# Kernel tuning notes

Hardware: AMD Instinct MI355X
Metric: run time of the kernel (lower is better)

Reference implementation:

```python
import jax, jax.numpy as jnp
import numpy as np
from jax import lax

STRIDE, PADDING, DILATION = 1, 1, 1


def setup_inputs() -> dict:
    key = jax.random.key(0)
    ks = jax.random.split(key, 6)
    B, C, H, W = 32, 128, 64, 64
    K, O, ksz = 4, 256, 3
    red = 32  # C // reduction
    # kaiming-ish scales
    return {
        "x": jax.random.normal(ks[0], (B, C, H, W), jnp.float32),
        "weights": jax.random.normal(ks[1], (K, O, C, ksz, ksz), jnp.float32) * (1.0 / np.sqrt(C * ksz * ksz)),
        "w1": jax.random.normal(ks[2], (red, C), jnp.float32) * (1.0 / np.sqrt(C)),
        "b1": jnp.zeros((red,), jnp.float32),
        "w2": jax.random.normal(ks[3], (K, red), jnp.float32) * (1.0 / np.sqrt(red)),
        "b2": jnp.zeros((K,), jnp.float32),
    }


def reference(x, weights, w1, b1, w2, b2):
    B, C, H, W = x.shape
    K, O, Cw, kh, kw = weights.shape
    # attention over kernels: global avg pool -> MLP -> softmax  [B, K]
    pooled = jnp.mean(x, axis=(2, 3))                       # [B, C]
    h = jax.nn.relu(pooled @ w1.T + b1)                     # [B, red]
    att = jax.nn.softmax(h @ w2.T + b2, axis=1)             # [B, K]
    # per-sample mixed kernel: [B, O, C, kh, kw]
    wk = jnp.einsum('bk,koihw->boihw', att, weights)
    # batched per-sample conv via grouped convolution (groups = B)
    lhs = x.reshape(1, B * C, H, W)
    rhs = wk.reshape(B * O, C, kh, kw)
    out = lax.conv_general_dilated(
        lhs, rhs,
        window_strides=(STRIDE, STRIDE),
        padding=[(PADDING, PADDING), (PADDING, PADDING)],
        rhs_dilation=(DILATION, DILATION),
        dimension_numbers=('NCHW', 'OIHW', 'NCHW'),
        feature_group_count=B,
    )
    Ho, Wo = out.shape[2], out.shape[3]
    return out.reshape(B, O, Ho, Wo)
```

## Files before the change

### kernel.cpp

```cpp
#include <hip/hip_runtime.h>
#include <math.h>

#define BB 32
#define CC 128
#define HH 64
#define WW 64
#define KK 4
#define OO 256
#define RED 32
#define HWSZ (HH*WW)
#define XT_W 66
#define GPLANE (XT_W*XT_W)

typedef __attribute__((ext_vector_type(8))) short bf16x8;
typedef __attribute__((ext_vector_type(4))) float f32x4;

static __device__ __forceinline__ unsigned short f2bf(float f) {
    unsigned int u = __float_as_uint(f);
    u += 0x7FFF + ((u >> 16) & 1);
    return (unsigned short)(u >> 16);
}

static __device__ __forceinline__ void async16(unsigned short* lds, const unsigned short* g) {
    __builtin_amdgcn_global_load_lds(
        (const __attribute__((address_space(1))) unsigned int*)g,
        (__attribute__((address_space(3))) unsigned int*)lds, 16, 0, 0);
}

__global__ __launch_bounds__(256) void transpose_pool(const float* __restrict__ x,
        unsigned short* __restrict__ xt, float* __restrict__ partial) {
    __shared__ float lt[CC][65];
    int h = blockIdx.x & 63;
    int b = blockIdx.x >> 6;
    const float* xb = x + ((size_t)b * CC * HH + h) * WW;
    for (int i = threadIdx.x; i < CC * 16; i += 256) {
        int c = i >> 4, f4 = i & 15;
        float4 v = *(const float4*)(xb + (size_t)c * HWSZ + f4 * 4);
        lt[c][f4 * 4 + 0] = v.x;
        lt[c][f4 * 4 + 1] = v.y;
        lt[c][f4 * 4 + 2] = v.z;
        lt[c][f4 * 4 + 3] = v.w;
    }
    __syncthreads();
    size_t bg = (size_t)b * 4;
    for (int i = threadIdx.x; i < 64 * 16; i += 256) {
        int ww = i >> 4, cs = i & 15;
        bf16x8 pk;
#pragma unroll
        for (int j = 0; j < 8; ++j) pk[j] = (short)f2bf(lt[cs * 8 + j][ww]);
        *(bf16x8*)&xt[(((bg + (cs >> 2)) * XT_W + (h + 1)) * XT_W + (ww + 1)) * 32 + (cs & 3) * 8] = pk;
    }
    if (threadIdx.x < 32) {
        int cs = threadIdx.x & 15;
        int col = (threadIdx.x < 16) ? 0 : 65;
        *(f32x4*)&xt[(((bg + (cs >> 2)) * XT_W + (h + 1)) * XT_W + col) * 32 + (cs & 3) * 8] =
            (f32x4){0.f, 0.f, 0.f, 0.f};
    }
    if (h == 0 || h == 63) {
        int hr = (h == 0) ? 0 : 65;
        for (int i = threadIdx.x; i < XT_W * 16; i += 256) {
            int px = i >> 4, cs = i & 15;
            *(f32x4*)&xt[(((bg + (cs >> 2)) * XT_W + hr) * XT_W + px) * 32 + (cs & 3) * 8] =
                (f32x4){0.f, 0.f, 0.f, 0.f};
        }
    }
    if (threadIdx.x < CC) {
        float s = 0.f;
#pragma unroll
        for (int j = 0; j < WW; ++j) s += lt[threadIdx.x][j];
        partial[(size_t)blockIdx.x * CC + threadIdx.x] = s;
    }
}

__global__ void att_kernel(const float* __restrict__ partial,
        const float* __restrict__ w1, const float* __restrict__ b1,
        const float* __restrict__ w2, const float* __restrict__ b2,
        float* __restrict__ att) {
    int b = blockIdx.x;
    int tid = threadIdx.x;
    __shared__ float ps[CC];
    __shared__ float hs[RED];
    __shared__ float ls[KK];
    if (tid < CC) {
        const float* pp = partial + (size_t)b * HH * CC + tid;
        float s = 0.f;
#pragma unroll
        for (int h = 0; h < HH; ++h) s += pp[(size_t)h * CC];
        ps[tid] = s * (1.0f / (float)HWSZ);
    }
    __syncthreads();
    int r = tid >> 3, j = tid & 7;
    const float* w1r = w1 + r * CC + j * 16;
    float p = 0.f;
#pragma unroll
    for (int c = 0; c < 16; ++c) p = fmaf(ps[j * 16 + c], w1r[c], p);
    p += __shfl_xor(p, 1, 64);
    p += __shfl_xor(p, 2, 64);
    p += __shfl_xor(p, 4, 64);
    if (j == 0) hs[r] = fmaxf(p + b1[r], 0.f);
    __syncthreads();
    if (tid < KK) {
        float acc = b2[tid];
        const float* w2k = w2 + tid * RED;
#pragma unroll
        for (int rr = 0; rr < RED; ++rr) acc = fmaf(hs[rr], w2k[rr], acc);
        ls[tid] = acc;
    }
    __syncthreads();
    if (tid == 0) {
        float m = fmaxf(fmaxf(ls[0], ls[1]), fmaxf(ls[2], ls[3]));
        float e0 = expf(ls[0] - m), e1 = expf(ls[1] - m);
        float e2 = expf(ls[2] - m), e3 = expf(ls[3] - m);
        float inv = 1.0f / (e0 + e1 + e2 + e3);
        att[b * KK + 0] = e0 * inv; att[b * KK + 1] = e1 * inv;
        att[b * KK + 2] = e2 * inv; att[b * KK + 3] = e3 * inv;
    }
}

__global__ __launch_bounds__(256) void mix_kernel(const float* __restrict__ w,
        const float* __restrict__ att, unsigned short* __restrict__ wk) {
    int gid = blockIdx.x * 256 + threadIdx.x;
    int c = gid & 127;
    int o = (gid >> 7) & 255;
    int b = gid >> 15;
    float a[KK];
#pragma unroll
    for (int k = 0; k < KK; ++k) a[k] = att[b * KK + k];
    float mixed[9];
#pragma unroll
    for (int t = 0; t < 9; ++t) mixed[t] = 0.f;
#pragma unroll
    for (int k = 0; k < KK; ++k) {
        const float* p = w + (((size_t)k * OO + o) * CC + c) * 9;
#pragma unroll
        for (int t = 0; t < 9; ++t) mixed[t] = fmaf(a[k], p[t], mixed[t]);
    }
    size_t base = ((size_t)b * 4 + (c >> 5)) * 9;
#pragma unroll
    for (int t = 0; t < 9; ++t)
        wk[((base + t) * OO + o) * 32 + (c & 31)] = f2bf(mixed[t]);
}

#define XS_C 32
#define AL_C 32
__global__ __launch_bounds__(256, 2) void conv_mfma(const unsigned short* __restrict__ xt,
        const unsigned short* __restrict__ wk, float* __restrict__ out) {
    __shared__ unsigned short xs[6 * XT_W * XS_C];
    __shared__ unsigned short als[2][128 * AL_C];

    int bid = blockIdx.x;
    int blk = (bid & 7) * 128 + (bid >> 3);
    int b  = blk >> 5;
    int rg = (blk >> 1) & 15;
    int ot = blk & 1;
    int r0 = rg * 4;
    int o0 = ot * 128;

    int tid = threadIdx.x;
    int lane = tid & 63;
    int wid = tid >> 6;
    int wm = wid & 1;
    int wn = wid >> 1;
    int l15 = lane & 15;
    int l4 = lane >> 4;

    f32x4 acc[4][8];
#pragma unroll
    for (int i = 0; i < 4; ++i)
#pragma unroll
        for (int j = 0; j < 8; ++j) acc[i][j] = (f32x4){0.f, 0.f, 0.f, 0.f};

    const unsigned short* xt_b = xt + (size_t)b * 4 * GPLANE * 32;
    const unsigned short* wk_b = wk + (size_t)b * 4 * 9 * OO * 32;

    for (int g = 0; g < 4; ++g) {
        __syncthreads();
        const unsigned short* xsrc = xt_b + ((size_t)g * GPLANE + r0 * XT_W) * 32;
        for (int i = tid; i < 1584; i += 256) {
            int pix = i >> 2, seg = i & 3;
            int segg = seg ^ ((pix >> 1) & 3);
            async16(xs + i * 8, xsrc + pix * 32 + segg * 8);
        }
        const unsigned short* wsrc = wk_b + ((size_t)g * 9 * OO + o0) * 32;
        {
            int ch = tid;
#pragma unroll
            for (int rep = 0; rep < 2; ++rep, ch += 256) {
                int o = ch >> 2, seg = ch & 3;
                int segg = seg ^ ((o >> 1) & 3);
                async16(als[0] + ch * 8, wsrc + o * 32 + segg * 8);
            }
        }
        __syncthreads();

        for (int t = 0; t < 9; ++t) {
            if (t < 8) {
                int ch = tid;
#pragma unroll
                for (int rep = 0; rep < 2; ++rep, ch += 256) {
                    int o = ch >> 2, seg = ch & 3;
                    int segg = seg ^ ((o >> 1) & 3);
                    async16(als[(t + 1) & 1] + ch * 8,
                            wsrc + ((size_t)(t + 1) * OO + o) * 32 + segg * 8);
                }
            }
            int kh = t / 3, kw = t - kh * 3;
            bf16x8 af[4], bfv[8];
#pragma unroll
            for (int mf = 0; mf < 4; ++mf) {
                int orow = wm * 64 + mf * 16 + l15;
                af[mf] = *(const bf16x8*)&als[t & 1][orow * AL_C + (l4 ^ ((orow >> 1) & 3)) * 8];
            }
#pragma unroll
            for (int nf = 0; nf < 8; ++nf) {
                int prow = wn * 2 + (nf >> 2) + kh;
                int pcol = (nf & 3) * 16 + l15 + kw;
                int pix = prow * XT_W + pcol;
                bfv[nf] = *(const bf16x8*)&xs[pix * XS_C + (l4 ^ ((pix >> 1) & 3)) * 8];
            }
#pragma unroll
            for (int mf = 0; mf < 4; ++mf)
#pragma unroll
                for (int nf = 0; nf < 8; ++nf)
                    acc[mf][nf] = __builtin_amdgcn_mfma_f32_16x16x32_bf16(
                        af[mf], bfv[nf], acc[mf][nf], 0, 0, 0);
            if (t < 8) __syncthreads();
        }
    }

    float* outb = out + ((size_t)b * OO + o0) * HWSZ;
#pragma unroll
    for (int mf = 0; mf < 4; ++mf)
#pragma unroll
        for (int nf = 0; nf < 8; ++nf) {
            int row = r0 + wn * 2 + (nf >> 2);
            int col = (nf & 3) * 16 + l15;
#pragma unroll
            for (int r = 0; r < 4; ++r) {
                int o = wm * 64 + mf * 16 + l4 * 4 + r;
                outb[(size_t)o * HWSZ + row * WW + col] = acc[mf][nf][r];
            }
        }
}

extern "C" void kernel_launch(void* const* d_in, const int* in_sizes, int n_in,
                              void* d_out, int out_size, void* d_ws, size_t ws_size,
                              hipStream_t stream) {
    const float* x       = (const float*)d_in[0];
    const float* weights = (const float*)d_in[1];
    const float* w1      = (const float*)d_in[2];
    const float* b1      = (const float*)d_in[3];
    const float* w2      = (const float*)d_in[4];
    const float* b2      = (const float*)d_in[5];
    float* out = (float*)d_out;

    char* ws = (char*)d_ws;
    float* partial      = (float*)ws;
    float* att          = (float*)(ws + 1048576);
    unsigned short* wk  = (unsigned short*)(ws + 1048576 + 4096);
    unsigned short* xtp = (unsigned short*)(ws + 1048576 + 4096 + 18874368);

    transpose_pool<<<BB * HH, 256, 0, stream>>>(x, xtp, partial);
    att_kernel<<<BB, 256, 0, stream>>>(partial, w1, b1, w2, b2, att);
    mix_kernel<<<BB * OO * CC / 256, 256, 0, stream>>>(weights, att, wk);
    conv_mfma<<<BB * 2 * 16, 256, 0, stream>>>(xtp, wk, out);
}
```

Baseline: 272.1 us.

## Load conv weights straight to registers and double-buffer input tile across groups

Weight fragments are no longer staged through LDS with per-tap barriers. Each wave now reads its A fragments directly from global memory, using a layout already grouped per 16 output channels. The input halo tile is double-buffered across the four channel groups, so only one barrier per group remains, and the MFMA block is wrapped in s_setprio. This removes most of the synchronisation and LDS traffic, at the cost of exposing global/L2 load latency on the weight reads in each tap.

```diff
diff --git a/kernel.cpp b/kernel.cpp
--- a/kernel.cpp
+++ b/kernel.cpp
@@ -142,11 +142,10 @@
 }
 
 #define XS_C 32
-#define AL_C 32
 __global__ __launch_bounds__(256, 2) void conv_mfma(const unsigned short* __restrict__ xt,
         const unsigned short* __restrict__ wk, float* __restrict__ out) {
-    __shared__ unsigned short xs[6 * XT_W * XS_C];
-    __shared__ unsigned short als[2][128 * AL_C];
+    __shared__ unsigned short xsA[6 * XT_W * XS_C];
+    __shared__ unsigned short xsB[6 * XT_W * XS_C];
 
     int bid = blockIdx.x;
     int blk = (bid & 7) * 128 + (bid >> 3);
@@ -171,62 +170,55 @@
         for (int j = 0; j < 8; ++j) acc[i][j] = (f32x4){0.f, 0.f, 0.f, 0.f};
 
     const unsigned short* xt_b = xt + (size_t)b * 4 * GPLANE * 32;
-    const unsigned short* wk_b = wk + (size_t)b * 4 * 9 * OO * 32;
-
-    for (int g = 0; g < 4; ++g) {
-        __syncthreads();
-        const unsigned short* xsrc = xt_b + ((size_t)g * GPLANE + r0 * XT_W) * 32;
-        for (int i = tid; i < 1584; i += 256) {
-            int pix = i >> 2, seg = i & 3;
-            int segg = seg ^ ((pix >> 1) & 3);
-            async16(xs + i * 8, xsrc + pix * 32 + segg * 8);
-        }
-        const unsigned short* wsrc = wk_b + ((size_t)g * 9 * OO + o0) * 32;
-        {
-            int ch = tid;
-#pragma unroll
-            for (int rep = 0; rep < 2; ++rep, ch += 256) {
-                int o = ch >> 2, seg = ch & 3;
-                int segg = seg ^ ((o >> 1) & 3);
-                async16(als[0] + ch * 8, wsrc + o * 32 + segg * 8);
-            }
-        }
-        __syncthreads();
-
-        for (int t = 0; t < 9; ++t) {
-            if (t < 8) {
-                int ch = tid;
-#pragma unroll
-                for (int rep = 0; rep < 2; ++rep, ch += 256) {
-                    int o = ch >> 2, seg = ch & 3;
-                    int segg = seg ^ ((o >> 1) & 3);
-                    async16(als[(t + 1) & 1] + ch * 8,
-                            wsrc + ((size_t)(t + 1) * OO + o) * 32 + segg * 8);
-                }
-            }
-            int kh = t / 3, kw = t - kh * 3;
-            bf16x8 af[4], bfv[8];
-#pragma unroll
-            for (int mf = 0; mf < 4; ++mf) {
-                int orow = wm * 64 + mf * 16 + l15;
-                af[mf] = *(const bf16x8*)&als[t & 1][orow * AL_C + (l4 ^ ((orow >> 1) & 3)) * 8];
-            }
-#pragma unroll
-            for (int nf = 0; nf < 8; ++nf) {
-                int prow = wn * 2 + (nf >> 2) + kh;
-                int pcol = (nf & 3) * 16 + l15 + kw;
-                int pix = prow * XT_W + pcol;
-                bfv[nf] = *(const bf16x8*)&xs[pix * XS_C + (l4 ^ ((pix >> 1) & 3)) * 8];
-            }
-#pragma unroll
-            for (int mf = 0; mf < 4; ++mf)
-#pragma unroll
-                for (int nf = 0; nf < 8; ++nf)
-                    acc[mf][nf] = __builtin_amdgcn_mfma_f32_16x16x32_bf16(
-                        af[mf], bfv[nf], acc[mf][nf], 0, 0, 0);
-            if (t < 8) __syncthreads();
-        }
-    }
+    const unsigned short* wk_w = wk +
+        ((size_t)b * 4 * 9 * OO + o0 + wm * 64 + l15) * 32 + l4 * 8;
+
+#define STAGE_XS(BUF, gidx) do {                                                  \
+    const unsigned short* xsrc = xt_b + ((size_t)(gidx) * GPLANE + r0 * XT_W) * 32; \
+    for (int i_ = tid; i_ < 1584; i_ += 256) {                                    \
+        int pix_ = i_ >> 2, seg_ = i_ & 3;                                        \
+        int segg_ = seg_ ^ ((pix_ >> 1) & 3);                                     \
+        async16((BUF) + i_ * 8, xsrc + pix_ * 32 + segg_ * 8);                    \
+    } } while (0)
+
+#define TAPS(BUF, gidx) do {                                                      \
+    _Pragma("unroll")                                                             \
+    for (int t = 0; t < 9; ++t) {                                                 \
+        int kh = t / 3, kw = t - kh * 3;                                          \
+        bf16x8 af[4], bfv[8];                                                     \
+        _Pragma("unroll")                                                         \
+        for (int mf = 0; mf < 4; ++mf)                                            \
+            af[mf] = *(const bf16x8*)(wk_w +                                      \
+                (((size_t)(gidx) * 9 + t) * OO + mf * 16) * 32);                  \
+        _Pragma("unroll")                                                         \
+        for (int nf = 0; nf < 8; ++nf) {                                          \
+            int prow = wn * 2 + (nf >> 2) + kh;                                   \
+            int pcol = (nf & 3) * 16 + l15 + kw;                                  \
+            int pix = prow * XT_W + pcol;                                         \
+            bfv[nf] = *(const bf16x8*)&(BUF)[pix * XS_C + (l4 ^ ((pix >> 1) & 3)) * 8]; \
+        }                                                                         \
+        __builtin_amdgcn_s_setprio(1);                                            \
+        _Pragma("unroll")                                                         \
+        for (int mf = 0; mf < 4; ++mf)                                            \
+            _Pragma("unroll")                                                     \
+            for (int nf = 0; nf < 8; ++nf)                                        \
+                acc[mf][nf] = __builtin_amdgcn_mfma_f32_16x16x32_bf16(            \
+                    af[mf], bfv[nf], acc[mf][nf], 0, 0, 0);                       \
+        __builtin_amdgcn_s_setprio(0);                                            \
+    } } while (0)
+
+    STAGE_XS(xsA, 0);
+    __syncthreads();
+    TAPS(xsA, 0); STAGE_XS(xsB, 1);
+    __syncthreads();
+    TAPS(xsB, 1); STAGE_XS(xsA, 2);
+    __syncthreads();
+    TAPS(xsA, 2); STAGE_XS(xsB, 3);
+    __syncthreads();
+    TAPS(xsB, 3);
+
+#undef STAGE_XS
+#undef TAPS
 
     float* outb = out + ((size_t)b * OO + o0) * HWSZ;
 #pragma unroll
```

Result: slower. 312.9 us (+15.0%).
